# Optimization experiments

Hardware: AMD Instinct MI355X
Metric: run time of the kernel (lower is better)

Reference implementation:

```python
import jax, jax.numpy as jnp
import numpy as np

EMBED_DIM, NUM_HEADS, LOCAL_SIZE = 256, 4, 15
HEAD_DIM = EMBED_DIM // NUM_HEADS
SCALING = float(HEAD_DIM) ** -0.5


def get_overlap_segments(x, window_size):
    # x: (n, t, d) -> (n, t, window_size, d), zero-padded local windows centered at each position
    n, t, d = x.shape
    p = (window_size - 1) // 2
    xp = jnp.pad(x, ((0, 0), (p, p), (0, 0)))
    idx = jnp.arange(t)[:, None] + jnp.arange(window_size)[None, :]  # (t, w)
    return xp[:, idx]


def setup_inputs():
    key = jax.random.key(0)
    ks = jax.random.split(key, 4)
    B, W, F = 4, 64, 4096
    T = W + F
    x = jax.random.normal(ks[0], (B, T, EMBED_DIM), dtype=jnp.float32)
    # block one-hot frame->window assignment (each window owns F//W consecutive frames)
    assign = jnp.repeat(jnp.arange(W), F // W)
    wm = jnp.broadcast_to(jax.nn.one_hot(assign, W, dtype=jnp.float32).T[None], (B, W, F))
    W_qkv = jax.random.normal(ks[1], (EMBED_DIM, 3 * EMBED_DIM), jnp.float32) * 0.02
    b_qkv = jnp.zeros((3 * EMBED_DIM,), jnp.float32)
    W_out = jax.random.normal(ks[2], (EMBED_DIM, EMBED_DIM), jnp.float32) * 0.02
    b_out = jnp.zeros((EMBED_DIM,), jnp.float32)
    return {"x": x, "window_mapping": wm, "W_qkv": W_qkv, "b_qkv": b_qkv,
            "W_out": W_out, "b_out": b_out}


def _to_heads(z, b, t):
    # (b, t, E) -> (b*H, t, d), matching torch transpose/reshape ordering (b outer, h inner)
    return z.reshape(b, t, NUM_HEADS, HEAD_DIM).transpose(0, 2, 1, 3).reshape(b * NUM_HEADS, t, HEAD_DIM)


def reference(x, window_mapping, W_qkv, b_qkv, W_out, b_out):
    b, t, e = x.shape
    Wn, Fn = window_mapping.shape[1], window_mapping.shape[2]
    qkv = x @ W_qkv + b_qkv
    Q, K, V = jnp.split(qkv, 3, axis=-1)
    Q = Q * SCALING
    wtok = _to_heads(x[:, :Wn], b, Wn)            # (n, W, d) raw word tokens
    Qh = _to_heads(Q, b, t)[:, Wn:]               # (n, F, d)
    Kh = _to_heads(K, b, t)[:, Wn:]
    Vh = _to_heads(V, b, t)[:, Wn:]
    wm = jnp.broadcast_to(window_mapping[:, None], (b, NUM_HEADS, Wn, Fn)).reshape(b * NUM_HEADS, Wn, Fn)
    # scatter each window's word token to its frames
    expa = jnp.einsum('nwd,nwf->nfd', wtok, wm)   # (n, F, d)
    Kseg = get_overlap_segments(Kh, LOCAL_SIZE)   # (n, F, w, d)
    Vseg = get_overlap_segments(Vh, LOCAL_SIZE)
    Kcat = jnp.concatenate([expa[:, :, None], Kseg], axis=2)  # (n, F, 1+w, d)
    scores = jnp.einsum('nfd,nfwd->nfw', Qh, Kcat)            # (n, F, 1+w)
    # word-token weight: softmax across frames within each window chunk (F % W == 0, no pad)
    chunk = Fn // Wn
    w_wtok = jax.nn.softmax(scores[:, :, 0].reshape(-1, Wn, chunk), axis=-1).reshape(-1, Fn)
    # local-window weights: softmax over the window axis
    w_fea = jax.nn.softmax(scores[:, :, 1:], axis=-1)
    attn = jnp.concatenate([w_wtok[:, :, None], w_fea], axis=2)  # (n, F, 1+w)
    Vcat = jnp.concatenate([expa[:, :, None], Vseg], axis=2)
    out_fea = jnp.einsum('nfw,nfwd->nfd', attn, Vcat)            # (n, F, d)
    out = jnp.concatenate([wtok, out_fea], axis=1)               # (n, T, d)
    out = out.reshape(b, NUM_HEADS, t, HEAD_DIM).transpose(0, 2, 1, 3).reshape(b, t, e)
    return out @ W_out + b_out
```

## Files before the change

### kernel.cpp

```cpp
#include <hip/hip_runtime.h>


#define QN 4194304ull

typedef _Float16 h8 __attribute__((ext_vector_type(8)));
typedef float f32x16 __attribute__((ext_vector_type(16)));

__global__ __launch_bounds__(256) void conv_small(
    const float* __restrict__ x, const float* __restrict__ wm,
    const float* __restrict__ Wq, const float* __restrict__ Wo,
    _Float16* __restrict__ wqth, _Float16* __restrict__ woth,
    _Float16* __restrict__ wmth, _Float16* __restrict__ xth) {
  __shared__ float S[64 * 65];
  const int g = blockIdx.x, tid = threadIdx.x;
  if (g < 768) {
    int o = g * 256 + tid;
    int n = o >> 8, k = o & 255;
    wqth[o] = (_Float16)Wq[(size_t)k * 768 + n];
  } else if (g < 1024) {
    int o = (g - 768) * 256 + tid;
    int n = o >> 8, k = o & 255;
    woth[o] = (_Float16)Wo[(size_t)k * 256 + n];
  } else if (g < 1280) {
    int local = g - 1024;
    int b = local >> 6, f0 = (local & 63) * 64;
    {
      int w = tid >> 2, c0 = (tid & 3) * 16;
      const float* src = wm + ((size_t)(b * 64 + w)) * 4096 + f0 + c0;
#pragma unroll
      for (int cc = 0; cc < 16; cc += 4)
        *(float4*)&S[w * 65 + c0 + cc] = *(const float4*)(src + cc);
    }
    __syncthreads();
    {
      int fl = tid >> 2, w0 = (tid & 3) * 16;
      int f = f0 + fl;
      _Float16 hh[16];
#pragma unroll
      for (int j = 0; j < 16; ++j) hh[j] = (_Float16)S[(w0 + j) * 65 + fl];
      size_t o = ((size_t)b * 4096 + f) * 64 + w0;
      *(float4*)(wmth + o) = *(float4*)&hh[0];
      *(float4*)(wmth + o + 8) = *(float4*)&hh[8];
    }
  } else {
    int local = g - 1280;
    int b = local;
    for (int c0 = 0; c0 < 256; c0 += 64) {
      __syncthreads();
      {
        int w = tid >> 2, cl0 = (tid & 3) * 16;
        const float* src = x + ((size_t)(b * 4160 + w)) * 256 + c0 + cl0;
#pragma unroll
        for (int cc = 0; cc < 16; cc += 4)
          *(float4*)&S[w * 65 + cl0 + cc] = *(const float4*)(src + cc);
      }
      __syncthreads();
      {
        int cl = tid >> 2, w0 = (tid & 3) * 16;
        _Float16 hh[16];
#pragma unroll
        for (int j = 0; j < 16; ++j) hh[j] = (_Float16)S[(w0 + j) * 65 + cl];
        size_t o = ((size_t)(b * 256 + c0 + cl)) * 64 + w0;
        *(float4*)(xth + o) = *(float4*)&hh[0];
        *(float4*)(xth + o + 8) = *(float4*)&hh[8];
      }
    }
  }
}

__global__ __launch_bounds__(256) void qkv_mfma(
    const float* __restrict__ x, const _Float16* __restrict__ wth,
    const float* __restrict__ bq,
    float* __restrict__ Qb, float* __restrict__ Kb, float* __restrict__ Vb) {
  __shared__ _Float16 Ah[128][40], Bh[128][40];
  const int tid = threadIdx.x;
  const int wave = tid >> 6, lane = tid & 63;
  const int ln = lane & 31, half = lane >> 5;
  const int mw = (wave & 1) * 64, nw = (wave >> 1) * 64;
  const int m0 = blockIdx.x * 128, n0 = blockIdx.y * 128;

  const int sr = tid >> 1, scq = (tid & 1) * 16;
  const int am = m0 + sr;
  const size_t arow =
      ((size_t)((am >> 12) * 4160 + 64 + (am & 4095))) * 256 + scq;
  const size_t brow = (size_t)(n0 + sr) * 256 + scq;

  float4 rah0, rah1, rbh0, rbh1;
  auto QLOAD = [&](int k0_) {
    float4 fx0 = *(const float4*)(x + arow + k0_);
    float4 fx1 = *(const float4*)(x + arow + k0_ + 4);
    float4 fx2 = *(const float4*)(x + arow + k0_ + 8);
    float4 fx3 = *(const float4*)(x + arow + k0_ + 12);
    rbh0 = *(const float4*)(wth + brow + k0_);
    rbh1 = *(const float4*)(wth + brow + k0_ + 8);
    _Float16 hh[16] = {
        (_Float16)fx0.x, (_Float16)fx0.y, (_Float16)fx0.z, (_Float16)fx0.w,
        (_Float16)fx1.x, (_Float16)fx1.y, (_Float16)fx1.z, (_Float16)fx1.w,
        (_Float16)fx2.x, (_Float16)fx2.y, (_Float16)fx2.z, (_Float16)fx2.w,
        (_Float16)fx3.x, (_Float16)fx3.y, (_Float16)fx3.z, (_Float16)fx3.w};
    rah0 = *(float4*)&hh[0];
    rah1 = *(float4*)&hh[8];
  };

  QLOAD(0);
  f32x16 acc[2][2] = {};

  for (int it = 0; it < 8; ++it) {
    __syncthreads();
    *(float4*)&Ah[sr][scq] = rah0;
    *(float4*)&Ah[sr][scq + 8] = rah1;
    *(float4*)&Bh[sr][scq] = rbh0;
    *(float4*)&Bh[sr][scq + 8] = rbh1;
    __syncthreads();
    if (it < 7) QLOAD((it + 1) * 32);
#pragma unroll
    for (int ks = 0; ks < 2; ++ks) {
      const int kc = ks * 16 + half * 8;
      h8 a0 = *(const h8*)&Ah[mw + ln][kc];
      h8 a1 = *(const h8*)&Ah[mw + 32 + ln][kc];
      h8 b0 = *(const h8*)&Bh[nw + ln][kc];
      h8 b1 = *(const h8*)&Bh[nw + 32 + ln][kc];
      acc[0][0] = __builtin_amdgcn_mfma_f32_32x32x16_f16(a0, b0, acc[0][0], 0, 0, 0);
      acc[0][1] = __builtin_amdgcn_mfma_f32_32x32x16_f16(a0, b1, acc[0][1], 0, 0, 0);
      acc[1][0] = __builtin_amdgcn_mfma_f32_32x32x16_f16(a1, b0, acc[1][0], 0, 0, 0);
      acc[1][1] = __builtin_amdgcn_mfma_f32_32x32x16_f16(a1, b1, acc[1][1], 0, 0, 0);
    }
  }

#pragma unroll
  for (int ni = 0; ni < 2; ++ni) {
    const int c = n0 + nw + ni * 32 + ln;
    const int which = c >> 8, e = c & 255;
    const int h = e >> 6, d = e & 63;
    float* dst = (which == 0) ? Qb : (which == 1) ? Kb : Vb;
    const float sc2 = (which == 0) ? 0.125f : 1.0f;
    const float bias = bq[c];
#pragma unroll
    for (int mi = 0; mi < 2; ++mi) {
      const int rb = m0 + mw + mi * 32 + 4 * half;
#pragma unroll
      for (int reg = 0; reg < 16; ++reg) {
        int rr = rb + (reg & 3) + 8 * (reg >> 2);
        int b2 = rr >> 12, f2 = rr & 4095;
        dst[(((size_t)(b2 * 4 + h)) * 4096 + f2) * 64 + d] =
            (acc[mi][ni][reg] + bias) * sc2;
      }
    }
  }
}

__global__ __launch_bounds__(256) void attn_fused(
    const float* __restrict__ Qb, const float* __restrict__ Kb,
    const float* __restrict__ Vb,
    const _Float16* __restrict__ wmth, const _Float16* __restrict__ xth,
    _Float16* __restrict__ OFh) {
  __shared__ float Ks[78][68];
  __shared__ float Vs[78][68];
  __shared__ float EXs[64][68];
  __shared__ float s0s[64];
  __shared__ float red[2];
  const int tid = threadIdx.x;
  const int w = blockIdx.x;
  const int n = blockIdx.y;
  const int f0 = w * 64;
  const int b = n >> 2, h = n & 3;

  for (int idx = tid; idx < 78 * 16; idx += 256) {
    int rr = idx >> 4, c = (idx & 15) * 4;
    int g = f0 - 7 + rr;
    float4 kv = {0.f, 0.f, 0.f, 0.f}, vv = {0.f, 0.f, 0.f, 0.f};
    if (g >= 0 && g < 4096) {
      size_t base = ((size_t)n * 4096 + g) * 64 + c;
      kv = *(const float4*)(Kb + base);
      vv = *(const float4*)(Vb + base);
    }
    *(float4*)&Ks[rr][c] = kv;
    *(float4*)&Vs[rr][c] = vv;
  }
  {
    const int wave = tid >> 6, lane = tid & 63;
    const int ln = lane & 31, half = lane >> 5;
    const int mi = wave & 1, ni = wave >> 1;
    const size_t arow = ((size_t)(b * 4096 + f0 + mi * 32 + ln)) * 64 + half * 8;
    const size_t brow =
        ((size_t)(b * 256 + h * 64 + ni * 32 + ln)) * 64 + half * 8;
    f32x16 eacc = {};
#pragma unroll
    for (int ks = 0; ks < 4; ++ks) {
      const int kc = ks * 16;
      h8 ah = *(const h8*)(wmth + arow + kc);
      h8 bh = *(const h8*)(xth + brow + kc);
      eacc = __builtin_amdgcn_mfma_f32_32x32x16_f16(ah, bh, eacc, 0, 0, 0);
    }
    const int col = ni * 32 + ln;
    const int rb2 = mi * 32 + 4 * half;
#pragma unroll
    for (int reg = 0; reg < 16; ++reg)
      EXs[rb2 + (reg & 3) + 8 * (reg >> 2)][col] = eacc[reg];
  }
  __syncthreads();

  const int i = tid >> 2, q = tid & 3;
  const int f = f0 + i;
  const size_t qbase = ((size_t)n * 4096 + f) * 64 + q * 16;
  float4 q0 = *(const float4*)(Qb + qbase);
  float4 q1 = *(const float4*)(Qb + qbase + 4);
  float4 q2 = *(const float4*)(Qb + qbase + 8);
  float4 q3 = *(const float4*)(Qb + qbase + 12);
  float4 e0 = *(const float4*)&EXs[i][q * 16];
  float4 e1 = *(const float4*)&EXs[i][q * 16 + 4];
  float4 e2 = *(const float4*)&EXs[i][q * 16 + 8];
  float4 e3 = *(const float4*)&EXs[i][q * 16 + 12];

  float s0 = q0.x * e0.x + q0.y * e0.y + q0.z * e0.z + q0.w * e0.w +
             q1.x * e1.x + q1.y * e1.y + q1.z * e1.z + q1.w * e1.w +
             q2.x * e2.x + q2.y * e2.y + q2.z * e2.z + q2.w * e2.w +
             q3.x * e3.x + q3.y * e3.y + q3.z * e3.z + q3.w * e3.w;
  s0 += __shfl_xor(s0, 1);
  s0 += __shfl_xor(s0, 2);

  float sj[15];
#pragma unroll
  for (int j = 0; j < 15; ++j) {
    const float* kr = &Ks[i + j][q * 16];
    float4 k0 = *(const float4*)(kr);
    float4 k1 = *(const float4*)(kr + 4);
    float4 k2 = *(const float4*)(kr + 8);
    float4 k3 = *(const float4*)(kr + 12);
    float s = q0.x * k0.x + q0.y * k0.y + q0.z * k0.z + q0.w * k0.w +
              q1.x * k1.x + q1.y * k1.y + q1.z * k1.z + q1.w * k1.w +
              q2.x * k2.x + q2.y * k2.y + q2.z * k2.z + q2.w * k2.w +
              q3.x * k3.x + q3.y * k3.y + q3.z * k3.z + q3.w * k3.w;
    s += __shfl_xor(s, 1);
    s += __shfl_xor(s, 2);
    sj[j] = s;
  }

  if (q == 0) s0s[i] = s0;
  __syncthreads();
  if (tid < 64) {
    float v = s0s[tid];
    float m = v;
    for (int o = 1; o < 64; o <<= 1) m = fmaxf(m, __shfl_xor(m, o));
    float ee = expf(v - m);
    float s = ee;
    for (int o = 1; o < 64; o <<= 1) s += __shfl_xor(s, o);
    if (tid == 0) { red[0] = m; red[1] = s; }
  }
  __syncthreads();
  const float wt = expf(s0 - red[0]) / red[1];

  float mx = sj[0];
#pragma unroll
  for (int j = 1; j < 15; ++j) mx = fmaxf(mx, sj[j]);
  float pj[15], den = 0.f;
#pragma unroll
  for (int j = 0; j < 15; ++j) { pj[j] = expf(sj[j] - mx); den += pj[j]; }
  const float inv = 1.0f / den;

  float o[16] = {wt * e0.x, wt * e0.y, wt * e0.z, wt * e0.w,
                 wt * e1.x, wt * e1.y, wt * e1.z, wt * e1.w,
                 wt * e2.x, wt * e2.y, wt * e2.z, wt * e2.w,
                 wt * e3.x, wt * e3.y, wt * e3.z, wt * e3.w};
#pragma unroll
  for (int j = 0; j < 15; ++j) {
    float wj = pj[j] * inv;
    const float* vr = &Vs[i + j][q * 16];
#pragma unroll
    for (int dd = 0; dd < 16; ++dd) o[dd] = fmaf(wj, vr[dd], o[dd]);
  }
  _Float16 oh[16];
#pragma unroll
  for (int dd = 0; dd < 16; ++dd) oh[dd] = (_Float16)o[dd];
  *(float4*)(OFh + qbase) = *(float4*)&oh[0];
  *(float4*)(OFh + qbase + 8) = *(float4*)&oh[8];
}

__global__ __launch_bounds__(256) void out_mfma(
    const float* __restrict__ x, const _Float16* __restrict__ ofh,
    const _Float16* __restrict__ wth, const float* __restrict__ bo,
    float* __restrict__ out) {
  __shared__ _Float16 Ah[64][72], Bh[64][72];
  const int tid = threadIdx.x;
  const int wave = tid >> 6, lane = tid & 63;
  const int ln = lane & 31, half = lane >> 5;
  const int mw = (wave & 1) * 32, nw = (wave >> 1) * 32;
  const int m0 = blockIdx.x * 64, n0 = blockIdx.y * 64;
  const int sr = tid >> 2, sc4 = (tid & 3) * 16;
  const int m = m0 + sr;
  const int b = m / 4160, tt = m % 4160;
  const bool useX = (tt < 64);
  const size_t xrow = ((size_t)(b * 4160 + tt)) * 256 + sc4;
  const long obase = ((long)(b * 4) * 4096 + (tt - 64)) * 64 + sc4;
  const size_t bbase = (size_t)(n0 + sr) * 256 + sc4;

  float4 ra0, ra1, rb0, rb1;
  auto OLOAD = [&](int k0_) {
    if (useX) {
      float4 fx0 = *(const float4*)(x + xrow + k0_);
      float4 fx1 = *(const float4*)(x + xrow + k0_ + 4);
      float4 fx2 = *(const float4*)(x + xrow + k0_ + 8);
      float4 fx3 = *(const float4*)(x + xrow + k0_ + 12);
      _Float16 hh[16] = {
          (_Float16)fx0.x, (_Float16)fx0.y, (_Float16)fx0.z, (_Float16)fx0.w,
          (_Float16)fx1.x, (_Float16)fx1.y, (_Float16)fx1.z, (_Float16)fx1.w,
          (_Float16)fx2.x, (_Float16)fx2.y, (_Float16)fx2.z, (_Float16)fx2.w,
          (_Float16)fx3.x, (_Float16)fx3.y, (_Float16)fx3.z, (_Float16)fx3.w};
      ra0 = *(float4*)&hh[0];
      ra1 = *(float4*)&hh[8];
    } else {
      size_t o_ = (size_t)(obase + (long)(k0_ >> 6) * 262144);
      ra0 = *(const float4*)(ofh + o_);
      ra1 = *(const float4*)(ofh + o_ + 8);
    }
    rb0 = *(const float4*)(wth + bbase + k0_);
    rb1 = *(const float4*)(wth + bbase + k0_ + 8);
  };

  OLOAD(0);
  f32x16 acc = {};
  for (int it = 0; it < 4; ++it) {
    __syncthreads();
    *(float4*)&Ah[sr][sc4] = ra0;
    *(float4*)&Ah[sr][sc4 + 8] = ra1;
    *(float4*)&Bh[sr][sc4] = rb0;
    *(float4*)&Bh[sr][sc4 + 8] = rb1;
    __syncthreads();
    if (it < 3) OLOAD((it + 1) * 64);
#pragma unroll
    for (int ks = 0; ks < 4; ++ks) {
      const int kc = ks * 16 + half * 8;
      h8 ah = *(const h8*)&Ah[mw + ln][kc];
      h8 bh = *(const h8*)&Bh[nw + ln][kc];
      acc = __builtin_amdgcn_mfma_f32_32x32x16_f16(ah, bh, acc, 0, 0, 0);
    }
  }
  const int c = n0 + nw + ln;
  const float bias = bo[c];
  const int rb = m0 + mw + 4 * half;
#pragma unroll
  for (int reg = 0; reg < 16; ++reg) {
    int rr = rb + (reg & 3) + 8 * (reg >> 2);
    out[(size_t)rr * 256 + c] = acc[reg] + bias;
  }
}

extern "C" void kernel_launch(void* const* d_in, const int* in_sizes, int n_in,
                              void* d_out, int out_size, void* d_ws, size_t ws_size,
                              hipStream_t stream) {
  const float* x  = (const float*)d_in[0];
  const float* wm = (const float*)d_in[1];
  const float* Wq = (const float*)d_in[2];
  const float* bq = (const float*)d_in[3];
  const float* Wo = (const float*)d_in[4];
  const float* bo = (const float*)d_in[5];
  float* out = (float*)d_out;
  float* ws = (float*)d_ws;

  float* Qb = ws;
  float* Kb = Qb + QN;
  float* Vb = Kb + QN;
  _Float16* OFh  = (_Float16*)(Vb + QN);
  _Float16* Wqth = OFh + QN;
  _Float16* Woth = Wqth + 196608;
  _Float16* wmTh = Woth + 65536;
  _Float16* xTh  = wmTh + 1048576;

  conv_small<<<dim3(1284), 256, 0, stream>>>(x, wm, Wq, Wo, Wqth, Woth, wmTh,
                                             xTh);
  qkv_mfma<<<dim3(128, 6), 256, 0, stream>>>(x, Wqth, bq, Qb, Kb, Vb);
  attn_fused<<<dim3(64, 16), 256, 0, stream>>>(Qb, Kb, Vb, wmTh, xTh, OFh);
  out_mfma<<<dim3(260, 4), 256, 0, stream>>>(x, OFh, Woth, bo, out);
}
```

Before: 127.4 us.

## Fuse QKV projection GEMM into conversion kernel, reading Wq directly

The separate Wq transpose/convert pass and the QKV GEMM kernel are merged into one launch. The GEMM blocks now load fp32 Wq straight from global memory with strided per-element reads and convert them in registers, while the remaining blocks still convert Wo, the window mapping and x. Shared memory is unioned between the GEMM tiles and the transpose buffer. This removes one kernel launch and the Wq half-precision round trip, at the cost of uncoalesced strided Wq loads inside the GEMM inner loop.

```diff
diff --git a/kernel.cpp b/kernel.cpp
--- a/kernel.cpp
+++ b/kernel.cpp
@@ -6,30 +6,111 @@
 typedef _Float16 h8 __attribute__((ext_vector_type(8)));
 typedef float f32x16 __attribute__((ext_vector_type(16)));
 
-__global__ __launch_bounds__(256) void conv_small(
+__global__ __launch_bounds__(256) void qkv_conv(
     const float* __restrict__ x, const float* __restrict__ wm,
     const float* __restrict__ Wq, const float* __restrict__ Wo,
-    _Float16* __restrict__ wqth, _Float16* __restrict__ woth,
-    _Float16* __restrict__ wmth, _Float16* __restrict__ xth) {
-  __shared__ float S[64 * 65];
-  const int g = blockIdx.x, tid = threadIdx.x;
-  if (g < 768) {
-    int o = g * 256 + tid;
-    int n = o >> 8, k = o & 255;
-    wqth[o] = (_Float16)Wq[(size_t)k * 768 + n];
-  } else if (g < 1024) {
-    int o = (g - 768) * 256 + tid;
+    const float* __restrict__ bq,
+    float* __restrict__ Qb, float* __restrict__ Kb, float* __restrict__ Vb,
+    _Float16* __restrict__ woth, _Float16* __restrict__ wmth,
+    _Float16* __restrict__ xth) {
+  __shared__ union {
+    struct { _Float16 Ah[128][40], Bh[128][40]; } g;
+    float S[64 * 65];
+  } sh;
+  const int tid = threadIdx.x;
+  const int u = blockIdx.x;
+
+  if (u < 768) {
+    const int wave = tid >> 6, lane = tid & 63;
+    const int ln = lane & 31, half = lane >> 5;
+    const int mw = (wave & 1) * 64, nw = (wave >> 1) * 64;
+    const int m0 = (u & 127) * 128, n0 = (u >> 7) * 128;
+
+    const int sr = tid >> 1, scq = (tid & 1) * 16;
+    const int am = m0 + sr;
+    const size_t arow =
+        ((size_t)((am >> 12) * 4160 + 64 + (am & 4095))) * 256 + scq;
+    const int bn = n0 + sr;
+
+    float4 rah0, rah1, rbh0, rbh1;
+    auto QLOAD = [&](int k0_) {
+      float4 fx0 = *(const float4*)(x + arow + k0_);
+      float4 fx1 = *(const float4*)(x + arow + k0_ + 4);
+      float4 fx2 = *(const float4*)(x + arow + k0_ + 8);
+      float4 fx3 = *(const float4*)(x + arow + k0_ + 12);
+      _Float16 hh[16] = {
+          (_Float16)fx0.x, (_Float16)fx0.y, (_Float16)fx0.z, (_Float16)fx0.w,
+          (_Float16)fx1.x, (_Float16)fx1.y, (_Float16)fx1.z, (_Float16)fx1.w,
+          (_Float16)fx2.x, (_Float16)fx2.y, (_Float16)fx2.z, (_Float16)fx2.w,
+          (_Float16)fx3.x, (_Float16)fx3.y, (_Float16)fx3.z, (_Float16)fx3.w};
+      rah0 = *(float4*)&hh[0];
+      rah1 = *(float4*)&hh[8];
+      _Float16 bb[16];
+#pragma unroll
+      for (int j = 0; j < 16; ++j)
+        bb[j] = (_Float16)Wq[(size_t)(k0_ + scq + j) * 768 + bn];
+      rbh0 = *(float4*)&bb[0];
+      rbh1 = *(float4*)&bb[8];
+    };
+
+    QLOAD(0);
+    f32x16 acc[2][2] = {};
+
+    for (int it = 0; it < 8; ++it) {
+      __syncthreads();
+      *(float4*)&sh.g.Ah[sr][scq] = rah0;
+      *(float4*)&sh.g.Ah[sr][scq + 8] = rah1;
+      *(float4*)&sh.g.Bh[sr][scq] = rbh0;
+      *(float4*)&sh.g.Bh[sr][scq + 8] = rbh1;
+      __syncthreads();
+      if (it < 7) QLOAD((it + 1) * 32);
+#pragma unroll
+      for (int ks = 0; ks < 2; ++ks) {
+        const int kc = ks * 16 + half * 8;
+        h8 a0 = *(const h8*)&sh.g.Ah[mw + ln][kc];
+        h8 a1 = *(const h8*)&sh.g.Ah[mw + 32 + ln][kc];
+        h8 b0 = *(const h8*)&sh.g.Bh[nw + ln][kc];
+        h8 b1 = *(const h8*)&sh.g.Bh[nw + 32 + ln][kc];
+        acc[0][0] = __builtin_amdgcn_mfma_f32_32x32x16_f16(a0, b0, acc[0][0], 0, 0, 0);
+        acc[0][1] = __builtin_amdgcn_mfma_f32_32x32x16_f16(a0, b1, acc[0][1], 0, 0, 0);
+        acc[1][0] = __builtin_amdgcn_mfma_f32_32x32x16_f16(a1, b0, acc[1][0], 0, 0, 0);
+        acc[1][1] = __builtin_amdgcn_mfma_f32_32x32x16_f16(a1, b1, acc[1][1], 0, 0, 0);
+      }
+    }
+
+#pragma unroll
+    for (int ni = 0; ni < 2; ++ni) {
+      const int c = n0 + nw + ni * 32 + ln;
+      const int which = c >> 8, e = c & 255;
+      const int h = e >> 6, d = e & 63;
+      float* dst = (which == 0) ? Qb : (which == 1) ? Kb : Vb;
+      const float sc2 = (which == 0) ? 0.125f : 1.0f;
+      const float bias = bq[c];
+#pragma unroll
+      for (int mi = 0; mi < 2; ++mi) {
+        const int rb = m0 + mw + mi * 32 + 4 * half;
+#pragma unroll
+        for (int reg = 0; reg < 16; ++reg) {
+          int rr = rb + (reg & 3) + 8 * (reg >> 2);
+          int b2 = rr >> 12, f2 = rr & 4095;
+          dst[(((size_t)(b2 * 4 + h)) * 4096 + f2) * 64 + d] =
+              (acc[mi][ni][reg] + bias) * sc2;
+        }
+      }
+    }
+  } else if (u < 1024) {
+    int o = (u - 768) * 256 + tid;
     int n = o >> 8, k = o & 255;
     woth[o] = (_Float16)Wo[(size_t)k * 256 + n];
-  } else if (g < 1280) {
-    int local = g - 1024;
+  } else if (u < 1280) {
+    int local = u - 1024;
     int b = local >> 6, f0 = (local & 63) * 64;
     {
       int w = tid >> 2, c0 = (tid & 3) * 16;
       const float* src = wm + ((size_t)(b * 64 + w)) * 4096 + f0 + c0;
 #pragma unroll
       for (int cc = 0; cc < 16; cc += 4)
-        *(float4*)&S[w * 65 + c0 + cc] = *(const float4*)(src + cc);
+        *(float4*)&sh.S[w * 65 + c0 + cc] = *(const float4*)(src + cc);
     }
     __syncthreads();
     {
@@ -37,14 +118,13 @@
       int f = f0 + fl;
       _Float16 hh[16];
 #pragma unroll
-      for (int j = 0; j < 16; ++j) hh[j] = (_Float16)S[(w0 + j) * 65 + fl];
+      for (int j = 0; j < 16; ++j) hh[j] = (_Float16)sh.S[(w0 + j) * 65 + fl];
       size_t o = ((size_t)b * 4096 + f) * 64 + w0;
       *(float4*)(wmth + o) = *(float4*)&hh[0];
       *(float4*)(wmth + o + 8) = *(float4*)&hh[8];
     }
   } else {
-    int local = g - 1280;
-    int b = local;
+    int b = u - 1280;
     for (int c0 = 0; c0 < 256; c0 += 64) {
       __syncthreads();
       {
@@ -52,98 +132,17 @@
         const float* src = x + ((size_t)(b * 4160 + w)) * 256 + c0 + cl0;
 #pragma unroll
         for (int cc = 0; cc < 16; cc += 4)
-          *(float4*)&S[w * 65 + cl0 + cc] = *(const float4*)(src + cc);
+          *(float4*)&sh.S[w * 65 + cl0 + cc] = *(const float4*)(src + cc);
       }
       __syncthreads();
       {
         int cl = tid >> 2, w0 = (tid & 3) * 16;
         _Float16 hh[16];
 #pragma unroll
-        for (int j = 0; j < 16; ++j) hh[j] = (_Float16)S[(w0 + j) * 65 + cl];
+        for (int j = 0; j < 16; ++j) hh[j] = (_Float16)sh.S[(w0 + j) * 65 + cl];
         size_t o = ((size_t)(b * 256 + c0 + cl)) * 64 + w0;
         *(float4*)(xth + o) = *(float4*)&hh[0];
         *(float4*)(xth + o + 8) = *(float4*)&hh[8];
-      }
-    }
-  }
-}
-
-__global__ __launch_bounds__(256) void qkv_mfma(
-    const float* __restrict__ x, const _Float16* __restrict__ wth,
-    const float* __restrict__ bq,
-    float* __restrict__ Qb, float* __restrict__ Kb, float* __restrict__ Vb) {
-  __shared__ _Float16 Ah[128][40], Bh[128][40];
-  const int tid = threadIdx.x;
-  const int wave = tid >> 6, lane = tid & 63;
-  const int ln = lane & 31, half = lane >> 5;
-  const int mw = (wave & 1) * 64, nw = (wave >> 1) * 64;
-  const int m0 = blockIdx.x * 128, n0 = blockIdx.y * 128;
-
-  const int sr = tid >> 1, scq = (tid & 1) * 16;
-  const int am = m0 + sr;
-  const size_t arow =
-      ((size_t)((am >> 12) * 4160 + 64 + (am & 4095))) * 256 + scq;
-  const size_t brow = (size_t)(n0 + sr) * 256 + scq;
-
-  float4 rah0, rah1, rbh0, rbh1;
-  auto QLOAD = [&](int k0_) {
-    float4 fx0 = *(const float4*)(x + arow + k0_);
-    float4 fx1 = *(const float4*)(x + arow + k0_ + 4);
-    float4 fx2 = *(const float4*)(x + arow + k0_ + 8);
-    float4 fx3 = *(const float4*)(x + arow + k0_ + 12);
-    rbh0 = *(const float4*)(wth + brow + k0_);
-    rbh1 = *(const float4*)(wth + brow + k0_ + 8);
-    _Float16 hh[16] = {
-        (_Float16)fx0.x, (_Float16)fx0.y, (_Float16)fx0.z, (_Float16)fx0.w,
-        (_Float16)fx1.x, (_Float16)fx1.y, (_Float16)fx1.z, (_Float16)fx1.w,
-        (_Float16)fx2.x, (_Float16)fx2.y, (_Float16)fx2.z, (_Float16)fx2.w,
-        (_Float16)fx3.x, (_Float16)fx3.y, (_Float16)fx3.z, (_Float16)fx3.w};
-    rah0 = *(float4*)&hh[0];
-    rah1 = *(float4*)&hh[8];
-  };
-
-  QLOAD(0);
-  f32x16 acc[2][2] = {};
-
-  for (int it = 0; it < 8; ++it) {
-    __syncthreads();
-    *(float4*)&Ah[sr][scq] = rah0;
-    *(float4*)&Ah[sr][scq + 8] = rah1;
-    *(float4*)&Bh[sr][scq] = rbh0;
-    *(float4*)&Bh[sr][scq + 8] = rbh1;
-    __syncthreads();
-    if (it < 7) QLOAD((it + 1) * 32);
-#pragma unroll
-    for (int ks = 0; ks < 2; ++ks) {
-      const int kc = ks * 16 + half * 8;
-      h8 a0 = *(const h8*)&Ah[mw + ln][kc];
-      h8 a1 = *(const h8*)&Ah[mw + 32 + ln][kc];
-      h8 b0 = *(const h8*)&Bh[nw + ln][kc];
-      h8 b1 = *(const h8*)&Bh[nw + 32 + ln][kc];
-      acc[0][0] = __builtin_amdgcn_mfma_f32_32x32x16_f16(a0, b0, acc[0][0], 0, 0, 0);
-      acc[0][1] = __builtin_amdgcn_mfma_f32_32x32x16_f16(a0, b1, acc[0][1], 0, 0, 0);
-      acc[1][0] = __builtin_amdgcn_mfma_f32_32x32x16_f16(a1, b0, acc[1][0], 0, 0, 0);
-      acc[1][1] = __builtin_amdgcn_mfma_f32_32x32x16_f16(a1, b1, acc[1][1], 0, 0, 0);
-    }
-  }
-
-#pragma unroll
-  for (int ni = 0; ni < 2; ++ni) {
-    const int c = n0 + nw + ni * 32 + ln;
-    const int which = c >> 8, e = c & 255;
-    const int h = e >> 6, d = e & 63;
-    float* dst = (which == 0) ? Qb : (which == 1) ? Kb : Vb;
-    const float sc2 = (which == 0) ? 0.125f : 1.0f;
-    const float bias = bq[c];
-#pragma unroll
-    for (int mi = 0; mi < 2; ++mi) {
-      const int rb = m0 + mw + mi * 32 + 4 * half;
-#pragma unroll
-      for (int reg = 0; reg < 16; ++reg) {
-        int rr = rb + (reg & 3) + 8 * (reg >> 2);
-        int b2 = rr >> 12, f2 = rr & 4095;
-        dst[(((size_t)(b2 * 4 + h)) * 4096 + f2) * 64 + d] =
-            (acc[mi][ni][reg] + bias) * sc2;
       }
     }
   }
@@ -361,14 +360,12 @@
   float* Kb = Qb + QN;
   float* Vb = Kb + QN;
   _Float16* OFh  = (_Float16*)(Vb + QN);
-  _Float16* Wqth = OFh + QN;
-  _Float16* Woth = Wqth + 196608;
+  _Float16* Woth = OFh + QN;
   _Float16* wmTh = Woth + 65536;
   _Float16* xTh  = wmTh + 1048576;
 
-  conv_small<<<dim3(1284), 256, 0, stream>>>(x, wm, Wq, Wo, Wqth, Woth, wmTh,
-                                             xTh);
-  qkv_mfma<<<dim3(128, 6), 256, 0, stream>>>(x, Wqth, bq, Qb, Kb, Vb);
+  qkv_conv<<<dim3(1284), 256, 0, stream>>>(x, wm, Wq, Wo, bq, Qb, Kb, Vb,
+                                           Woth, wmTh, xTh);
   attn_fused<<<dim3(64, 16), 256, 0, stream>>>(Qb, Kb, Vb, wmTh, xTh, OFh);
   out_mfma<<<dim3(260, 4), 256, 0, stream>>>(x, OFh, Woth, bo, out);
 }
```

New measurement: 129.8 us. Within noise of the previous version (+1.8%).
